# Kernel tuning notes

Hardware: AMD Instinct MI355X
Metric: run time of the kernel (lower is better)

Reference implementation:

```python
import jax, jax.numpy as jnp
import numpy as np

K = 5
TAU = 2.0
EPS = 1e-8
SLOPE = 0.2  # LeakyReLU negative slope
BASE = jnp.array([-2.0, -1.0, 0.0, 1.0, 2.0], dtype=jnp.float32)


def _leaky(x):
    return jnp.where(x >= 0, x, SLOPE * x)


def _bilinear1d(feat, x):
    """1D bilinear sample, equivalent to F.grid_sample on an [B,C,1,L] image
    with grid_y=0, padding_mode='border', align_corners=True.
    feat: [B,C,L], x: [B,M] normalized coords in [-1,1]. Returns [B,C,M]."""
    L = feat.shape[-1]
    ix = jnp.clip((x + 1.0) * 0.5 * (L - 1), 0.0, float(L - 1))  # border clamp
    x0 = jnp.floor(ix)
    w = (ix - x0)[:, None, :]  # [B,1,M]
    i0 = jnp.clip(x0.astype(jnp.int32), 0, L - 1)
    i1 = jnp.clip(i0 + 1, 0, L - 1)
    f0 = jnp.take_along_axis(feat, i0[:, None, :], axis=2)
    f1 = jnp.take_along_axis(feat, i1[:, None, :], axis=2)
    return f0 * (1.0 - w) + f1 * w


def setup_inputs() -> dict:
    key = jax.random.key(0)
    ks = jax.random.split(key, 10)
    B, C, Lin, N, H = 4, 256, 4096, 8192, 64
    out_dim = 1 + 1 + K + K  # 12
    feat_1d = jax.random.normal(ks[0], (B, C, Lin), dtype=jnp.float32)
    coords_1d = jax.random.uniform(ks[1], (B, N, 1), minval=-1.0, maxval=1.0, dtype=jnp.float32)
    cell_1d = jnp.full((B, N, 1), 2.0 / Lin, dtype=jnp.float32) * (1.0 + 0.1 * jax.random.uniform(ks[2], (B, N, 1)))
    in_dim = C + 2
    # NOTE: original zero-inits the last linear; we use small random weights to
    # exercise the full computation (non-degenerate offsets/gates).
    W1 = jax.random.normal(ks[3], (in_dim, H), dtype=jnp.float32) * (1.0 / np.sqrt(in_dim))
    b1 = jax.random.normal(ks[4], (H,), dtype=jnp.float32) * 0.01
    Wr = jax.random.normal(ks[5], (H, H), dtype=jnp.float32) * (1.0 / np.sqrt(H))
    br = jax.random.normal(ks[6], (H,), dtype=jnp.float32) * 0.01
    W3 = jax.random.normal(ks[7], (H, out_dim), dtype=jnp.float32) * 0.1
    b3 = jax.random.normal(ks[8], (out_dim,), dtype=jnp.float32) * 0.01
    return {"feat_1d": feat_1d, "coords_1d": coords_1d, "cell_1d": cell_1d,
            "W1": W1, "b1": b1, "Wr": Wr, "br": br, "W3": W3, "b3": b3}


def reference(feat_1d, coords_1d, cell_1d, W1, b1, Wr, br, W3, b3):
    B, C, Lin = feat_1d.shape
    N = coords_1d.shape[1]
    x = coords_1d[..., 0]  # [B,N]
    # anchor features at query coords
    f_anchor = _bilinear1d(feat_1d, x).transpose(0, 2, 1)  # [B,N,C]
    rin = jnp.concatenate([f_anchor, coords_1d, cell_1d], axis=-1)  # [B,N,C+2]
    # router MLP: Linear -> LeakyReLU -> ResidualBlock -> Linear
    h = _leaky(rin @ W1 + b1)
    h = _leaky(h + (h @ Wr + br))
    out = h @ W3 + b3  # [B,N,12]
    r_raw = out[..., 0:1]
    sigma_raw = out[..., 1:2]
    res_raw = out[..., 2:2 + K]
    gate_raw = out[..., 2 + K:2 + 2 * K]
    r = jnp.clip(jax.nn.softplus(r_raw) + 0.3, 0.3, 2.0)          # [B,N,1]
    sigma = jnp.clip(jax.nn.softplus(sigma_raw) + 0.5, 0.5, 3.0)  # [B,N,1]
    res = jnp.tanh(res_raw) * 0.5                                  # [B,N,K]
    off = r * BASE + res                                           # [B,N,K] pixel-unit offsets
    scale_x = 2.0 / max(Lin - 1, 1)
    deform_x = x[:, :, None] + off * scale_x                       # [B,N,K] normalized
    f = _bilinear1d(feat_1d, deform_x.reshape(B, N * K))           # [B,C,N*K]
    f = f.reshape(B, C, N, K).transpose(0, 2, 3, 1)                # [B,N,K,C]
    w_geo = jnp.exp(-0.5 * off ** 2 / ((sigma * TAU) ** 2 + EPS))  # [B,N,K]
    w = w_geo * jax.nn.sigmoid(gate_raw)
    w = w / (w.sum(axis=-1, keepdims=True) + EPS)
    out_feat = jnp.einsum('bnkc,bnk->bnc', f, w)                   # [B,N,C]
    return out_feat
```

## Files before the change

kernel.cpp:

```cpp
#include <hip/hip_runtime.h>
#include <math.h>

#define KK 5
#define C_DIM 256
#define LIN 4096
#define B_DIM 4
#define N_PTS 8192
#define PTS 32
#define NBUCK (B_DIM * LIN)
#define WROWS 32
#define SROWS 44
#define WPB (LIN / WROWS)

typedef short short8 __attribute__((ext_vector_type(8)));
typedef float f32x4  __attribute__((ext_vector_type(4)));

__device__ __forceinline__ float leaky(float v) { return v >= 0.0f ? v : 0.2f * v; }
__device__ __forceinline__ float softplus_f(float v) { return v > 20.0f ? v : log1pf(expf(v)); }
__device__ __forceinline__ float bflo(unsigned u) { return __uint_as_float(u << 16); }
__device__ __forceinline__ float bfhi(unsigned u) { return __uint_as_float(u & 0xFFFF0000u); }
__device__ __forceinline__ ushort f2bf(float f) {
    unsigned u = __float_as_uint(f);
    u += 0x7FFFu + ((u >> 16) & 1u);
    return (ushort)(u >> 16);
}
__device__ __forceinline__ float bf2f(ushort h) { return __uint_as_float((unsigned)h << 16); }
__device__ __forceinline__ int anchor_key(const float* coords, int pt) {
    float x = coords[pt];
    float ix = fminf(fmaxf((x + 1.0f) * 0.5f * (float)(LIN - 1), 0.0f), (float)(LIN - 1));
    return (pt >> 13) * LIN + (int)ix;
}

__global__ __launch_bounds__(256) void prep_weights(
    const float* __restrict__ W1, const float* __restrict__ Wr,
    ushort* __restrict__ W1t_hi, ushort* __restrict__ W1t_lo,
    ushort* __restrict__ Wrt_hi, ushort* __restrict__ Wrt_lo)
{
    int i = blockIdx.x * 256 + threadIdx.x;
    if (i < 64 * 264) {
        int j = i / 264, k = i % 264;
        float v = (k < 256) ? W1[(size_t)k * 64 + j] : 0.0f;
        ushort hi = f2bf(v);
        W1t_hi[i] = hi;
        W1t_lo[i] = f2bf(v - bf2f(hi));
    } else {
        int i2 = i - 64 * 264;
        if (i2 < 64 * 72) {
            int j = i2 / 72, k = i2 % 72;
            float v = (k < 64) ? Wr[(size_t)k * 64 + j] : 0.0f;
            ushort hi = f2bf(v);
            Wrt_hi[i2] = hi;
            Wrt_lo[i2] = f2bf(v - bf2f(hi));
        }
    }
}

__global__ __launch_bounds__(256) void sort_count(
    const float* __restrict__ coords, unsigned* __restrict__ hist)
{
    int pt = blockIdx.x * 256 + threadIdx.x;
    atomicAdd(&hist[anchor_key(coords, pt)], 1u);
}

__global__ __launch_bounds__(256) void sort_scan(
    const unsigned* __restrict__ hist, unsigned* __restrict__ offs,
    unsigned* __restrict__ pfx)
{
    __shared__ unsigned base[256];
    int t = threadIdx.x;
    unsigned s = 0;
    for (int i = 0; i < NBUCK / 256; i++) s += hist[t * (NBUCK / 256) + i];
    base[t] = s;
    __syncthreads();
    if (t == 0) {
        unsigned run = 0;
        for (int i = 0; i < 256; i++) { unsigned v = base[i]; base[i] = run; run += v; }
    }
    __syncthreads();
    unsigned run = base[t];
    for (int i = 0; i < NBUCK / 256; i++) {
        int idx = t * (NBUCK / 256) + i;
        offs[idx] = run;
        pfx[idx] = run;
        run += hist[idx];
    }
    if (t == 255) pfx[NBUCK] = run;
}

__global__ __launch_bounds__(256) void sort_scatter(
    const float* __restrict__ coords, unsigned* __restrict__ offs,
    int* __restrict__ perm)
{
    int pt = blockIdx.x * 256 + threadIdx.x;
    unsigned pos = atomicAdd(&offs[anchor_key(coords, pt)], 1u);
    perm[pos] = pt;
}

__global__ __launch_bounds__(256) void fused_kernel(
    const float* __restrict__ feat,
    const float* __restrict__ coords,
    const float* __restrict__ cell,
    const float* __restrict__ W1, const float* __restrict__ b1,
    const float* __restrict__ br,
    const float* __restrict__ W3, const float* __restrict__ b3,
    const ushort* __restrict__ W1t_hi, const ushort* __restrict__ W1t_lo,
    const ushort* __restrict__ Wrt_hi, const ushort* __restrict__ Wrt_lo,
    const int* __restrict__ perm, const unsigned* __restrict__ pfx,
    float* __restrict__ out)
{
    __shared__ ushort fs[SROWS][264];
    __shared__ ushort Ah[PTS][264], Al[PTS][264];
    __shared__ ushort H1h[PTS][72], H1l[PTS][72];
    __shared__ float  H2[PTS][68];
    __shared__ float  outs[PTS][12];
    __shared__ float  sxw[PTS][10];
    __shared__ float  xs[PTS], cls[PTS];
    __shared__ int    pts[PTS];

    const int t = threadIdx.x;
    const int b  = blockIdx.x / WPB;
    const int w0 = (blockIdx.x % WPB) * WROWS;
    const int rowLo = max(0, w0 - 5);
    const int rowHi = min(LIN, w0 + WROWS + 6);
    const int nrows = rowHi - rowLo;

    {
        const float* fsrc = feat + ((size_t)b * C_DIM + t) * LIN + rowLo;
        for (int l = 0; l < nrows; l++)
            fs[l][t] = f2bf(fsrc[l]);
    }

    const unsigned ptStart = pfx[b * LIN + w0];
    const unsigned ptEnd   = pfx[b * LIN + w0 + WROWS];

    const int wave = t >> 6, lane = t & 63;
    const int cr = lane & 15;
    const int kb = lane >> 4;
    const int jcol = wave * 16 + cr;
    const float wx  = W1[(size_t)256 * 64 + jcol];
    const float wc  = W1[(size_t)257 * 64 + jcol];
    const float bb1 = b1[jcol];
    const float brv = br[jcol];

    for (unsigned chunkBase = ptStart; chunkBase < ptEnd; chunkBase += PTS) {
        const int npts = (int)min((unsigned)PTS, ptEnd - chunkBase);
        __syncthreads();
        if (t < PTS) pts[t] = perm[chunkBase + min(t, npts - 1)];
        __syncthreads();

        {
            int p = t >> 3, l8 = t & 7;
            int pt = pts[p];
            float x = coords[pt];
            float ix = fminf(fmaxf((x + 1.0f) * 0.5f * (float)(LIN - 1), 0.0f), (float)(LIN - 1));
            float x0 = floorf(ix);
            int i0 = min((int)x0, LIN - 1);
            int i1 = min(i0 + 1, LIN - 1);
            float fr = ix - x0, om = 1.0f - fr;
            int r0 = i0 - rowLo, r1 = i1 - rowLo;
            if (l8 == 0) { xs[p] = x; cls[p] = cell[pt]; }
#pragma unroll
            for (int q = 0; q < 4; q++) {
                int c = l8 * 8 + q * 64;
                uint4 u0 = *(const uint4*)&fs[r0][c];
                uint4 u1 = *(const uint4*)&fs[r1][c];
                float v[8];
                v[0] = bflo(u0.x) * om + bflo(u1.x) * fr;
                v[1] = bfhi(u0.x) * om + bfhi(u1.x) * fr;
                v[2] = bflo(u0.y) * om + bflo(u1.y) * fr;
                v[3] = bfhi(u0.y) * om + bfhi(u1.y) * fr;
                v[4] = bflo(u0.z) * om + bflo(u1.z) * fr;
                v[5] = bfhi(u0.z) * om + bfhi(u1.z) * fr;
                v[6] = bflo(u0.w) * om + bflo(u1.w) * fr;
                v[7] = bfhi(u0.w) * om + bfhi(u1.w) * fr;
                ushort hv[8], lv[8];
#pragma unroll
                for (int e = 0; e < 8; e++) {
                    hv[e] = f2bf(v[e]);
                    lv[e] = f2bf(v[e] - bf2f(hv[e]));
                }
                *(uint4*)&Ah[p][c] = *(uint4*)hv;
                *(uint4*)&Al[p][c] = *(uint4*)lv;
            }
        }
        __syncthreads();

        f32x4 acc0 = {0.f, 0.f, 0.f, 0.f}, acc1 = acc0;
        {
            const ushort* B1h = W1t_hi + (size_t)jcol * 264;
            const ushort* B1l = W1t_lo + (size_t)jcol * 264;
#pragma unroll
            for (int k0 = 0; k0 < 256; k0 += 32) {
                int ko = k0 + kb * 8;
                short8 a0h = *(const short8*)&Ah[cr][ko];
                short8 a0l = *(const short8*)&Al[cr][ko];
                short8 a1h = *(const short8*)&Ah[16 + cr][ko];
                short8 a1l = *(const short8*)&Al[16 + cr][ko];
                short8 bh = *(const short8*)(B1h + ko);
                short8 bl = *(const short8*)(B1l + ko);
                acc0 = __builtin_amdgcn_mfma_f32_16x16x32_bf16(a0h, bh, acc0, 0, 0, 0);
                acc0 = __builtin_amdgcn_mfma_f32_16x16x32_bf16(a0h, bl, acc0, 0, 0, 0);
                acc0 = __builtin_amdgcn_mfma_f32_16x16x32_bf16(a0l, bh, acc0, 0, 0, 0);
                acc1 = __builtin_amdgcn_mfma_f32_16x16x32_bf16(a1h, bh, acc1, 0, 0, 0);
                acc1 = __builtin_amdgcn_mfma_f32_16x16x32_bf16(a1h, bl, acc1, 0, 0, 0);
                acc1 = __builtin_amdgcn_mfma_f32_16x16x32_bf16(a1l, bh, acc1, 0, 0, 0);
            }
        }
        float h1a[4], h1b[4];
#pragma unroll
        for (int r = 0; r < 4; r++) {
            int p0 = kb * 4 + r;
            float v0 = leaky(acc0[r] + xs[p0] * wx + cls[p0] * wc + bb1);
            h1a[r] = v0;
            ushort hi0 = f2bf(v0);
            H1h[p0][jcol] = hi0;
            H1l[p0][jcol] = f2bf(v0 - bf2f(hi0));
            int p1 = 16 + p0;
            float v1 = leaky(acc1[r] + xs[p1] * wx + cls[p1] * wc + bb1);
            h1b[r] = v1;
            ushort hi1 = f2bf(v1);
            H1h[p1][jcol] = hi1;
            H1l[p1][jcol] = f2bf(v1 - bf2f(hi1));
        }
        __syncthreads();

        {
            f32x4 r0 = {0.f, 0.f, 0.f, 0.f}, r1 = r0;
            const ushort* B2h = Wrt_hi + (size_t)jcol * 72;
            const ushort* B2l = Wrt_lo + (size_t)jcol * 72;
#pragma unroll
            for (int k0 = 0; k0 < 64; k0 += 32) {
                int ko = k0 + kb * 8;
                short8 a0h = *(const short8*)&H1h[cr][ko];
                short8 a0l = *(const short8*)&H1l[cr][ko];
                short8 a1h = *(const short8*)&H1h[16 + cr][ko];
                short8 a1l = *(const short8*)&H1l[16 + cr][ko];
                short8 bh = *(const short8*)(B2h + ko);
                short8 bl = *(const short8*)(B2l + ko);
                r0 = __builtin_amdgcn_mfma_f32_16x16x32_bf16(a0h, bh, r0, 0, 0, 0);
                r0 = __builtin_amdgcn_mfma_f32_16x16x32_bf16(a0h, bl, r0, 0, 0, 0);
                r0 = __builtin_amdgcn_mfma_f32_16x16x32_bf16(a0l, bh, r0, 0, 0, 0);
                r1 = __builtin_amdgcn_mfma_f32_16x16x32_bf16(a1h, bh, r1, 0, 0, 0);
                r1 = __builtin_amdgcn_mfma_f32_16x16x32_bf16(a1h, bl, r1, 0, 0, 0);
                r1 = __builtin_amdgcn_mfma_f32_16x16x32_bf16(a1l, bh, r1, 0, 0, 0);
            }
#pragma unroll
            for (int r = 0; r < 4; r++) {
                int p0 = kb * 4 + r;
                H2[p0][jcol]      = leaky(h1a[r] + r0[r] + brv);
                H2[16 + p0][jcol] = leaky(h1b[r] + r1[r] + brv);
            }
        }
        __syncthreads();

        {
            int p = t & 31;
            int o = t >> 5;
            for (int oo = o; oo < 12; oo += 8) {
                float acc = b3[oo];
#pragma unroll 4
                for (int l = 0; l < 64; l++)
                    acc = fmaf(H2[p][l], W3[(size_t)l * 12 + oo], acc);
                outs[p][oo] = acc;
            }
        }
        __syncthreads();

        if (t < PTS) {
            float x = xs[t];
            float r = softplus_f(outs[t][0]) + 0.3f;
            r = fminf(fmaxf(r, 0.3f), 2.0f);
            float sg = softplus_f(outs[t][1]) + 0.5f;
            sg = fminf(fmaxf(sg, 0.5f), 3.0f);
            float denom = (sg * 2.0f) * (sg * 2.0f) + 1e-8f;
            const float BASEv[KK] = {-2.0f, -1.0f, 0.0f, 1.0f, 2.0f};
            float wk[KK];
            float wsum = 0.0f;
#pragma unroll
            for (int k = 0; k < KK; k++) {
                float res = tanhf(outs[t][2 + k]) * 0.5f;
                float off = r * BASEv[k] + res;
                float dx = x + off * (2.0f / (float)(LIN - 1));
                float ix = (dx + 1.0f) * 0.5f * (float)(LIN - 1);
                ix = fminf(fmaxf(ix, 0.0f), (float)(LIN - 1));
                float gate = outs[t][2 + KK + k];
                float wgeo = expf(-0.5f * off * off / denom);
                float sig = 1.0f / (1.0f + expf(-gate));
                float w = wgeo * sig;
                sxw[t][k] = ix;
                wk[k] = w; wsum += w;
            }
            float inv = 1.0f / (wsum + 1e-8f);
#pragma unroll
            for (int k = 0; k < KK; k++) sxw[t][5 + k] = wk[k] * inv;
        }
        __syncthreads();

        {
            int worker = t >> 5, gl = t & 31;
            int c = gl * 8;
            for (int p = worker; p < npts; p += 8) {
                int pt = pts[p];
                float a0 = 0, a1 = 0, a2 = 0, a3 = 0, a4 = 0, a5 = 0, a6 = 0, a7 = 0;
#pragma unroll
                for (int k = 0; k < KK; k++) {
                    float ix = sxw[p][k];
                    float w  = sxw[p][5 + k];
                    float x0 = floorf(ix);
                    int i0 = (int)x0;
                    int i1 = min(i0 + 1, LIN - 1);
                    float fr = ix - x0;
                    uint4 u0 = *(const uint4*)&fs[i0 - rowLo][c];
                    uint4 u1 = *(const uint4*)&fs[i1 - rowLo][c];
                    float w0f = w * (1.0f - fr), w1f = w * fr;
                    a0 = fmaf(w0f, bflo(u0.x), fmaf(w1f, bflo(u1.x), a0));
                    a1 = fmaf(w0f, bfhi(u0.x), fmaf(w1f, bfhi(u1.x), a1));
                    a2 = fmaf(w0f, bflo(u0.y), fmaf(w1f, bflo(u1.y), a2));
                    a3 = fmaf(w0f, bfhi(u0.y), fmaf(w1f, bfhi(u1.y), a3));
                    a4 = fmaf(w0f, bflo(u0.z), fmaf(w1f, bflo(u1.z), a4));
                    a5 = fmaf(w0f, bfhi(u0.z), fmaf(w1f, bfhi(u1.z), a5));
                    a6 = fmaf(w0f, bflo(u0.w), fmaf(w1f, bflo(u1.w), a6));
                    a7 = fmaf(w0f, bfhi(u0.w), fmaf(w1f, bfhi(u1.w), a7));
                }
                float* op = out + (size_t)pt * C_DIM + c;
                *(float4*)op       = make_float4(a0, a1, a2, a3);
                *(float4*)(op + 4) = make_float4(a4, a5, a6, a7);
            }
        }
    }
}

extern "C" void kernel_launch(void* const* d_in, const int* in_sizes, int n_in,
                              void* d_out, int out_size, void* d_ws, size_t ws_size,
                              hipStream_t stream) {
    const float* feat   = (const float*)d_in[0];
    const float* coords = (const float*)d_in[1];
    const float* cell   = (const float*)d_in[2];
    const float* W1 = (const float*)d_in[3];
    const float* b1 = (const float*)d_in[4];
    const float* Wr = (const float*)d_in[5];
    const float* br = (const float*)d_in[6];
    const float* W3 = (const float*)d_in[7];
    const float* b3 = (const float*)d_in[8];
    float* out = (float*)d_out;

    char* ws = (char*)d_ws;
    ushort* W1t_hi = (ushort*)ws; ws += 64 * 264 * 2;
    ushort* W1t_lo = (ushort*)ws; ws += 64 * 264 * 2;
    ushort* Wrt_hi = (ushort*)ws; ws += 64 * 72 * 2;
    ushort* Wrt_lo = (ushort*)ws; ws += 64 * 72 * 2;
    ws = (char*)(((uintptr_t)ws + 255) & ~(uintptr_t)255);
    unsigned* hist = (unsigned*)ws; ws += NBUCK * 4;
    unsigned* offs = (unsigned*)ws; ws += NBUCK * 4;
    unsigned* pfx  = (unsigned*)ws; ws += (NBUCK + 1) * 4;
    ws = (char*)(((uintptr_t)ws + 255) & ~(uintptr_t)255);
    int* perm      = (int*)ws;      ws += (size_t)B_DIM * N_PTS * 4;

    int nPts = B_DIM * N_PTS;

    hipMemsetAsync(hist, 0, NBUCK * 4, stream);
    sort_count<<<nPts / 256, 256, 0, stream>>>(coords, hist);
    sort_scan<<<1, 256, 0, stream>>>(hist, offs, pfx);
    sort_scatter<<<nPts / 256, 256, 0, stream>>>(coords, offs, perm);

    prep_weights<<<(64 * 264 + 64 * 72 + 255) / 256, 256, 0, stream>>>(
        W1, Wr, W1t_hi, W1t_lo, Wrt_hi, Wrt_lo);

    fused_kernel<<<B_DIM * WPB, 256, 0, stream>>>(
        feat, coords, cell, W1, b1, br, W3, b3,
        W1t_hi, W1t_lo, Wrt_hi, Wrt_lo, perm, pfx, out);
}
```

Before: 148.4 us.

## Precompute first-layer GEMM on window rows and interpolate, coarsen sort buckets

Bilinear interpolation commutes with the first linear layer, so the first-layer MFMA GEMM now runs once per window on the stored feature rows. Each point then linearly interpolates the per-row results instead of running the 256-wide GEMM per point chunk. Windows shrink to 16 rows, which doubles the block count, and the sort now buckets by window with a merged scan+scatter kernel and fewer launches. LDS rows are padded and stored as hi/lo bf16 pairs. This adds a per-window GEMM whose cost is wasted on sparse windows, and the single-block scatter serialises 32K atomics.

After: 178.9 us. 20.6% more time.

```diff
diff --git a/kernel.cpp b/kernel.cpp
--- a/kernel.cpp
+++ b/kernel.cpp
@@ -7,36 +7,47 @@
 #define B_DIM 4
 #define N_PTS 8192
 #define PTS 32
-#define NBUCK (B_DIM * LIN)
-#define WROWS 32
-#define SROWS 44
+#define WROWS 16
 #define WPB (LIN / WROWS)
+#define NWIN (B_DIM * WPB)
+#define SROWS 28
+#define FS_STRIDE 268
+#define H1_STRIDE 76
+#define H2_STRIDE 67
+#define G_STRIDE 68
 
 typedef short short8 __attribute__((ext_vector_type(8)));
+typedef short short4v __attribute__((ext_vector_type(4)));
 typedef float f32x4  __attribute__((ext_vector_type(4)));
 
 __device__ __forceinline__ float leaky(float v) { return v >= 0.0f ? v : 0.2f * v; }
 __device__ __forceinline__ float softplus_f(float v) { return v > 20.0f ? v : log1pf(expf(v)); }
-__device__ __forceinline__ float bflo(unsigned u) { return __uint_as_float(u << 16); }
-__device__ __forceinline__ float bfhi(unsigned u) { return __uint_as_float(u & 0xFFFF0000u); }
 __device__ __forceinline__ ushort f2bf(float f) {
     unsigned u = __float_as_uint(f);
     u += 0x7FFFu + ((u >> 16) & 1u);
     return (ushort)(u >> 16);
 }
 __device__ __forceinline__ float bf2f(ushort h) { return __uint_as_float((unsigned)h << 16); }
-__device__ __forceinline__ int anchor_key(const float* coords, int pt) {
-    float x = coords[pt];
-    float ix = fminf(fmaxf((x + 1.0f) * 0.5f * (float)(LIN - 1), 0.0f), (float)(LIN - 1));
-    return (pt >> 13) * LIN + (int)ix;
-}
-
-__global__ __launch_bounds__(256) void prep_weights(
+
+__device__ __forceinline__ short8 lds_ld8(const ushort* p) {
+    union { short8 s8; short4v s4[2]; } u;
+    u.s4[0] = *(const short4v*)p;
+    u.s4[1] = *(const short4v*)(p + 4);
+    return u.s8;
+}
+
+__global__ __launch_bounds__(256) void prep_zero(
     const float* __restrict__ W1, const float* __restrict__ Wr,
     ushort* __restrict__ W1t_hi, ushort* __restrict__ W1t_lo,
-    ushort* __restrict__ Wrt_hi, ushort* __restrict__ Wrt_lo)
+    ushort* __restrict__ Wrt_hi, ushort* __restrict__ Wrt_lo,
+    unsigned* __restrict__ hist)
 {
-    int i = blockIdx.x * 256 + threadIdx.x;
+    int blk = blockIdx.x, t = threadIdx.x;
+    if (blk == 84) {
+        for (int i = t; i < NWIN; i += 256) hist[i] = 0u;
+        return;
+    }
+    int i = blk * 256 + t;
     if (i < 64 * 264) {
         int j = i / 264, k = i % 264;
         float v = (k < 256) ? W1[(size_t)k * 64 + j] : 0.0f;
@@ -58,209 +69,214 @@
 __global__ __launch_bounds__(256) void sort_count(
     const float* __restrict__ coords, unsigned* __restrict__ hist)
 {
-    int pt = blockIdx.x * 256 + threadIdx.x;
-    atomicAdd(&hist[anchor_key(coords, pt)], 1u);
-}
-
-__global__ __launch_bounds__(256) void sort_scan(
-    const unsigned* __restrict__ hist, unsigned* __restrict__ offs,
-    unsigned* __restrict__ pfx)
+    int gid = blockIdx.x * 256 + threadIdx.x;
+#pragma unroll
+    for (int i = 0; i < 4; i++) {
+        int pt = i * 8192 + gid;
+        float x = coords[pt];
+        float ix = fminf(fmaxf((x + 1.0f) * 0.5f * (float)(LIN - 1), 0.0f), (float)(LIN - 1));
+        int key = (pt >> 13) * WPB + ((int)ix >> 4);
+        atomicAdd(&hist[key], 1u);
+    }
+}
+
+__global__ __launch_bounds__(256) void scan_scatter(
+    const float* __restrict__ coords, const unsigned* __restrict__ hist,
+    unsigned* __restrict__ pfx, int* __restrict__ perm)
 {
-    __shared__ unsigned base[256];
+    __shared__ unsigned a[256];
+    __shared__ unsigned offs[NWIN];
     int t = threadIdx.x;
-    unsigned s = 0;
-    for (int i = 0; i < NBUCK / 256; i++) s += hist[t * (NBUCK / 256) + i];
-    base[t] = s;
+    unsigned h0 = hist[4 * t], h1 = hist[4 * t + 1];
+    unsigned h2 = hist[4 * t + 2], h3 = hist[4 * t + 3];
+    unsigned tsum = h0 + h1 + h2 + h3;
+    a[t] = tsum;
     __syncthreads();
-    if (t == 0) {
-        unsigned run = 0;
-        for (int i = 0; i < 256; i++) { unsigned v = base[i]; base[i] = run; run += v; }
-    }
+    for (int d = 1; d < 256; d <<= 1) {
+        unsigned v = (t >= d) ? a[t - d] : 0u;
+        __syncthreads();
+        a[t] += v;
+        __syncthreads();
+    }
+    unsigned ex = a[t] - tsum;
+    offs[4 * t]     = ex;
+    offs[4 * t + 1] = ex + h0;
+    offs[4 * t + 2] = ex + h0 + h1;
+    offs[4 * t + 3] = ex + h0 + h1 + h2;
+    pfx[4 * t]     = offs[4 * t];
+    pfx[4 * t + 1] = offs[4 * t + 1];
+    pfx[4 * t + 2] = offs[4 * t + 2];
+    pfx[4 * t + 3] = offs[4 * t + 3];
+    if (t == 255) pfx[NWIN] = a[255];
     __syncthreads();
-    unsigned run = base[t];
-    for (int i = 0; i < NBUCK / 256; i++) {
-        int idx = t * (NBUCK / 256) + i;
-        offs[idx] = run;
-        pfx[idx] = run;
-        run += hist[idx];
-    }
-    if (t == 255) pfx[NBUCK] = run;
-}
-
-__global__ __launch_bounds__(256) void sort_scatter(
-    const float* __restrict__ coords, unsigned* __restrict__ offs,
-    int* __restrict__ perm)
-{
-    int pt = blockIdx.x * 256 + threadIdx.x;
-    unsigned pos = atomicAdd(&offs[anchor_key(coords, pt)], 1u);
-    perm[pos] = pt;
-}
-
-__global__ __launch_bounds__(256) void fused_kernel(
-    const float* __restrict__ feat,
-    const float* __restrict__ coords,
+#pragma unroll 4
+    for (int i = 0; i < (B_DIM * N_PTS) / 256; i++) {
+        int pt = i * 256 + t;
+        float x = coords[pt];
+        float ix = fminf(fmaxf((x + 1.0f) * 0.5f * (float)(LIN - 1), 0.0f), (float)(LIN - 1));
+        int key = (pt >> 13) * WPB + ((int)ix >> 4);
+        unsigned pos = atomicAdd(&offs[key], 1u);
+        perm[pos] = pt;
+    }
+}
+
+__global__ __launch_bounds__(256, 3) void fused_kernel(
+    const float* __restrict__ feat, const float* __restrict__ coords,
     const float* __restrict__ cell,
     const float* __restrict__ W1, const float* __restrict__ b1,
-    const float* __restrict__ br,
-    const float* __restrict__ W3, const float* __restrict__ b3,
+    const float* __restrict__ br, const float* __restrict__ W3,
+    const float* __restrict__ b3,
     const ushort* __restrict__ W1t_hi, const ushort* __restrict__ W1t_lo,
     const ushort* __restrict__ Wrt_hi, const ushort* __restrict__ Wrt_lo,
     const int* __restrict__ perm, const unsigned* __restrict__ pfx,
     float* __restrict__ out)
 {
-    __shared__ ushort fs[SROWS][264];
-    __shared__ ushort Ah[PTS][264], Al[PTS][264];
-    __shared__ ushort H1h[PTS][72], H1l[PTS][72];
-    __shared__ float  H2[PTS][68];
+    __shared__ ushort fsh[SROWS * FS_STRIDE];
+    __shared__ __align__(16) char fslG_raw[SROWS * FS_STRIDE * 2];
+    ushort* fsl = (ushort*)fslG_raw;
+    float*  G   = (float*)fslG_raw;
+    __shared__ ushort H1h[PTS * H1_STRIDE], H1l[PTS * H1_STRIDE];
+    __shared__ float  H2[PTS * H2_STRIDE];
     __shared__ float  outs[PTS][12];
     __shared__ float  sxw[PTS][10];
-    __shared__ float  xs[PTS], cls[PTS];
-    __shared__ int    pts[PTS];
+    __shared__ float  xs[PTS], cls[PTS], frs[PTS];
+    __shared__ int    r0s[PTS], r1s[PTS], pts[PTS];
 
     const int t = threadIdx.x;
-    const int b  = blockIdx.x / WPB;
-    const int w0 = (blockIdx.x % WPB) * WROWS;
+    const int b   = blockIdx.x >> 8;
+    const int win = blockIdx.x & 255;
+    const int w0  = win * WROWS;
     const int rowLo = max(0, w0 - 5);
     const int rowHi = min(LIN, w0 + WROWS + 6);
     const int nrows = rowHi - rowLo;
 
     {
         const float* fsrc = feat + ((size_t)b * C_DIM + t) * LIN + rowLo;
-        for (int l = 0; l < nrows; l++)
-            fs[l][t] = f2bf(fsrc[l]);
-    }
-
-    const unsigned ptStart = pfx[b * LIN + w0];
-    const unsigned ptEnd   = pfx[b * LIN + w0 + WROWS];
-
-    const int wave = t >> 6, lane = t & 63;
-    const int cr = lane & 15;
-    const int kb = lane >> 4;
-    const int jcol = wave * 16 + cr;
-    const float wx  = W1[(size_t)256 * 64 + jcol];
-    const float wc  = W1[(size_t)257 * 64 + jcol];
-    const float bb1 = b1[jcol];
+#pragma unroll 4
+        for (int l = 0; l < nrows; l++) {
+            float v = fsrc[l];
+            ushort hi = f2bf(v);
+            fsh[l * FS_STRIDE + t] = hi;
+            fsl[l * FS_STRIDE + t] = f2bf(v - bf2f(hi));
+        }
+    }
+    __syncthreads();
+
+    const int lane = t & 63;
+    const int cr = lane & 15, kb = lane >> 4;
+    const int jcol = (t >> 6) * 16 + cr;
+
+    {
+        const int rA0 = min(cr, nrows - 1);
+        const int rA1 = min(16 + cr, nrows - 1);
+        const ushort* B1h = W1t_hi + (size_t)jcol * 264;
+        const ushort* B1l = W1t_lo + (size_t)jcol * 264;
+        f32x4 g0 = {0.f, 0.f, 0.f, 0.f}, g1 = g0;
+#pragma unroll
+        for (int k0 = 0; k0 < 256; k0 += 32) {
+            int ko = k0 + kb * 8;
+            short8 a0h = lds_ld8(fsh + rA0 * FS_STRIDE + ko);
+            short8 a0l = lds_ld8(fsl + rA0 * FS_STRIDE + ko);
+            short8 a1h = lds_ld8(fsh + rA1 * FS_STRIDE + ko);
+            short8 a1l = lds_ld8(fsl + rA1 * FS_STRIDE + ko);
+            short8 bh = *(const short8*)(B1h + ko);
+            short8 bl = *(const short8*)(B1l + ko);
+            g0 = __builtin_amdgcn_mfma_f32_16x16x32_bf16(a0h, bh, g0, 0, 0, 0);
+            g0 = __builtin_amdgcn_mfma_f32_16x16x32_bf16(a0h, bl, g0, 0, 0, 0);
+            g0 = __builtin_amdgcn_mfma_f32_16x16x32_bf16(a0l, bh, g0, 0, 0, 0);
+            g1 = __builtin_amdgcn_mfma_f32_16x16x32_bf16(a1h, bh, g1, 0, 0, 0);
+            g1 = __builtin_amdgcn_mfma_f32_16x16x32_bf16(a1h, bl, g1, 0, 0, 0);
+            g1 = __builtin_amdgcn_mfma_f32_16x16x32_bf16(a1l, bh, g1, 0, 0, 0);
+        }
+        __syncthreads();
+#pragma unroll
+        for (int r = 0; r < 4; r++) {
+            G[(kb * 4 + r) * G_STRIDE + jcol]        = g0[r];
+            G[(16 + kb * 4 + r) * G_STRIDE + jcol]   = g1[r];
+        }
+    }
+
+    const unsigned ptStart = pfx[b * WPB + win];
+    const unsigned ptEnd   = pfx[b * WPB + win + 1];
     const float brv = br[jcol];
 
-    for (unsigned chunkBase = ptStart; chunkBase < ptEnd; chunkBase += PTS) {
-        const int npts = (int)min((unsigned)PTS, ptEnd - chunkBase);
-        __syncthreads();
-        if (t < PTS) pts[t] = perm[chunkBase + min(t, npts - 1)];
-        __syncthreads();
-
-        {
-            int p = t >> 3, l8 = t & 7;
-            int pt = pts[p];
+    for (unsigned cb0 = ptStart; cb0 < ptEnd; cb0 += PTS) {
+        const int npts = (int)min((unsigned)PTS, ptEnd - cb0);
+        __syncthreads();
+        if (t < PTS) {
+            int pt = perm[cb0 + min(t, npts - 1)];
+            pts[t] = pt;
             float x = coords[pt];
             float ix = fminf(fmaxf((x + 1.0f) * 0.5f * (float)(LIN - 1), 0.0f), (float)(LIN - 1));
-            float x0 = floorf(ix);
-            int i0 = min((int)x0, LIN - 1);
+            float x0f = floorf(ix);
+            int i0 = min((int)x0f, LIN - 1);
             int i1 = min(i0 + 1, LIN - 1);
-            float fr = ix - x0, om = 1.0f - fr;
-            int r0 = i0 - rowLo, r1 = i1 - rowLo;
-            if (l8 == 0) { xs[p] = x; cls[p] = cell[pt]; }
-#pragma unroll
-            for (int q = 0; q < 4; q++) {
-                int c = l8 * 8 + q * 64;
-                uint4 u0 = *(const uint4*)&fs[r0][c];
-                uint4 u1 = *(const uint4*)&fs[r1][c];
-                float v[8];
-                v[0] = bflo(u0.x) * om + bflo(u1.x) * fr;
-                v[1] = bfhi(u0.x) * om + bfhi(u1.x) * fr;
-                v[2] = bflo(u0.y) * om + bflo(u1.y) * fr;
-                v[3] = bfhi(u0.y) * om + bfhi(u1.y) * fr;
-                v[4] = bflo(u0.z) * om + bflo(u1.z) * fr;
-                v[5] = bfhi(u0.z) * om + bfhi(u1.z) * fr;
-                v[6] = bflo(u0.w) * om + bflo(u1.w) * fr;
-                v[7] = bfhi(u0.w) * om + bfhi(u1.w) * fr;
-                ushort hv[8], lv[8];
-#pragma unroll
-                for (int e = 0; e < 8; e++) {
-                    hv[e] = f2bf(v[e]);
-                    lv[e] = f2bf(v[e] - bf2f(hv[e]));
-                }
-                *(uint4*)&Ah[p][c] = *(uint4*)hv;
-                *(uint4*)&Al[p][c] = *(uint4*)lv;
-            }
-        }
-        __syncthreads();
-
-        f32x4 acc0 = {0.f, 0.f, 0.f, 0.f}, acc1 = acc0;
+            r0s[t] = i0 - rowLo; r1s[t] = i1 - rowLo;
+            frs[t] = ix - x0f; xs[t] = x; cls[t] = cell[pt];
+        }
+        __syncthreads();
+
         {
-            const ushort* B1h = W1t_hi + (size_t)jcol * 264;
-            const ushort* B1l = W1t_lo + (size_t)jcol * 264;
-#pragma unroll
-            for (int k0 = 0; k0 < 256; k0 += 32) {
-                int ko = k0 + kb * 8;
-                short8 a0h = *(const short8*)&Ah[cr][ko];
-                short8 a0l = *(const short8*)&Al[cr][ko];
-                short8 a1h = *(const short8*)&Ah[16 + cr][ko];
-                short8 a1l = *(const short8*)&Al[16 + cr][ko];
-                short8 bh = *(const short8*)(B1h + ko);
-                short8 bl = *(const short8*)(B1l + ko);
-                acc0 = __builtin_amdgcn_mfma_f32_16x16x32_bf16(a0h, bh, acc0, 0, 0, 0);
-                acc0 = __builtin_amdgcn_mfma_f32_16x16x32_bf16(a0h, bl, acc0, 0, 0, 0);
-                acc0 = __builtin_amdgcn_mfma_f32_16x16x32_bf16(a0l, bh, acc0, 0, 0, 0);
-                acc1 = __builtin_amdgcn_mfma_f32_16x16x32_bf16(a1h, bh, acc1, 0, 0, 0);
-                acc1 = __builtin_amdgcn_mfma_f32_16x16x32_bf16(a1h, bl, acc1, 0, 0, 0);
-                acc1 = __builtin_amdgcn_mfma_f32_16x16x32_bf16(a1l, bh, acc1, 0, 0, 0);
-            }
-        }
-        float h1a[4], h1b[4];
-#pragma unroll
-        for (int r = 0; r < 4; r++) {
-            int p0 = kb * 4 + r;
-            float v0 = leaky(acc0[r] + xs[p0] * wx + cls[p0] * wc + bb1);
-            h1a[r] = v0;
-            ushort hi0 = f2bf(v0);
-            H1h[p0][jcol] = hi0;
-            H1l[p0][jcol] = f2bf(v0 - bf2f(hi0));
-            int p1 = 16 + p0;
-            float v1 = leaky(acc1[r] + xs[p1] * wx + cls[p1] * wc + bb1);
-            h1b[r] = v1;
-            ushort hi1 = f2bf(v1);
-            H1h[p1][jcol] = hi1;
-            H1l[p1][jcol] = f2bf(v1 - bf2f(hi1));
+            int p = t >> 3, j0 = (t & 7) * 8;
+            float fr = frs[p], om = 1.0f - fr;
+            float xv = xs[p], cv = cls[p];
+            const float* g0p = G + r0s[p] * G_STRIDE + j0;
+            const float* g1p = G + r1s[p] * G_STRIDE + j0;
+            const float* wxp = W1 + (size_t)256 * 64 + j0;
+            const float* wcp = W1 + (size_t)257 * 64 + j0;
+            const float* b1p = b1 + j0;
+            ushort* hh = H1h + p * H1_STRIDE + j0;
+            ushort* hl = H1l + p * H1_STRIDE + j0;
+#pragma unroll
+            for (int e = 0; e < 8; e++) {
+                float h = om * g0p[e] + fr * g1p[e] + xv * wxp[e] + cv * wcp[e] + b1p[e];
+                h = leaky(h);
+                ushort hi = f2bf(h);
+                hh[e] = hi;
+                hl[e] = f2bf(h - bf2f(hi));
+            }
         }
         __syncthreads();
 
         {
-            f32x4 r0 = {0.f, 0.f, 0.f, 0.f}, r1 = r0;
             const ushort* B2h = Wrt_hi + (size_t)jcol * 72;
             const ushort* B2l = Wrt_lo + (size_t)jcol * 72;
+            f32x4 r0a = {0.f, 0.f, 0.f, 0.f}, r1a = r0a;
 #pragma unroll
             for (int k0 = 0; k0 < 64; k0 += 32) {
                 int ko = k0 + kb * 8;
-                short8 a0h = *(const short8*)&H1h[cr][ko];
-                short8 a0l = *(const short8*)&H1l[cr][ko];
-                short8 a1h = *(const short8*)&H1h[16 + cr][ko];
-                short8 a1l = *(const short8*)&H1l[16 + cr][ko];
+                short8 a0h = lds_ld8(H1h + cr * H1_STRIDE + ko);
+                short8 a0l = lds_ld8(H1l + cr * H1_STRIDE + ko);
+                short8 a1h = lds_ld8(H1h + (16 + cr) * H1_STRIDE + ko);
+                short8 a1l = lds_ld8(H1l + (16 + cr) * H1_STRIDE + ko);
                 short8 bh = *(const short8*)(B2h + ko);
                 short8 bl = *(const short8*)(B2l + ko);
-                r0 = __builtin_amdgcn_mfma_f32_16x16x32_bf16(a0h, bh, r0, 0, 0, 0);
-                r0 = __builtin_amdgcn_mfma_f32_16x16x32_bf16(a0h, bl, r0, 0, 0, 0);
-                r0 = __builtin_amdgcn_mfma_f32_16x16x32_bf16(a0l, bh, r0, 0, 0, 0);
-                r1 = __builtin_amdgcn_mfma_f32_16x16x32_bf16(a1h, bh, r1, 0, 0, 0);
-                r1 = __builtin_amdgcn_mfma_f32_16x16x32_bf16(a1h, bl, r1, 0, 0, 0);
-                r1 = __builtin_amdgcn_mfma_f32_16x16x32_bf16(a1l, bh, r1, 0, 0, 0);
+                r0a = __builtin_amdgcn_mfma_f32_16x16x32_bf16(a0h, bh, r0a, 0, 0, 0);
+                r0a = __builtin_amdgcn_mfma_f32_16x16x32_bf16(a0h, bl, r0a, 0, 0, 0);
+                r0a = __builtin_amdgcn_mfma_f32_16x16x32_bf16(a0l, bh, r0a, 0, 0, 0);
+                r1a = __builtin_amdgcn_mfma_f32_16x16x32_bf16(a1h, bh, r1a, 0, 0, 0);
+                r1a = __builtin_amdgcn_mfma_f32_16x16x32_bf16(a1h, bl, r1a, 0, 0, 0);
+                r1a = __builtin_amdgcn_mfma_f32_16x16x32_bf16(a1l, bh, r1a, 0, 0, 0);
             }
 #pragma unroll
             for (int r = 0; r < 4; r++) {
                 int p0 = kb * 4 + r;
-                H2[p0][jcol]      = leaky(h1a[r] + r0[r] + brv);
-                H2[16 + p0][jcol] = leaky(h1b[r] + r1[r] + brv);
+                float h1v0 = bf2f(H1h[p0 * H1_STRIDE + jcol]) + bf2f(H1l[p0 * H1_STRIDE + jcol]);
+                H2[p0 * H2_STRIDE + jcol] = leaky(h1v0 + r0a[r] + brv);
+                int p1 = 16 + p0;
+                float h1v1 = bf2f(H1h[p1 * H1_STRIDE + jcol]) + bf2f(H1l[p1 * H1_STRIDE + jcol]);
+                H2[p1 * H2_STRIDE + jcol] = leaky(h1v1 + r1a[r] + brv);
             }
         }
         __syncthreads();
 
         {
-            int p = t & 31;
-            int o = t >> 5;
+            int p = t & 31, o = t >> 5;
             for (int oo = o; oo < 12; oo += 8) {
                 float acc = b3[oo];
-#pragma unroll 4
+#pragma unroll 8
                 for (int l = 0; l < 64; l++)
-                    acc = fmaf(H2[p][l], W3[(size_t)l * 12 + oo], acc);
+                    acc = fmaf(H2[p * H2_STRIDE + l], W3[(size_t)l * 12 + oo], acc);
                 outs[p][oo] = acc;
             }
         }
@@ -297,30 +313,33 @@
         __syncthreads();
 
         {
-            int worker = t >> 5, gl = t & 31;
+            int wg = t >> 5, gl = t & 31;
             int c = gl * 8;
-            for (int p = worker; p < npts; p += 8) {
+            for (int p = wg; p < npts; p += 8) {
                 int pt = pts[p];
                 float a0 = 0, a1 = 0, a2 = 0, a3 = 0, a4 = 0, a5 = 0, a6 = 0, a7 = 0;
 #pragma unroll
                 for (int k = 0; k < KK; k++) {
                     float ix = sxw[p][k];
                     float w  = sxw[p][5 + k];
-                    float x0 = floorf(ix);
-                    int i0 = (int)x0;
-                    int i1 = min(i0 + 1, LIN - 1);
-                    float fr = ix - x0;
-                    uint4 u0 = *(const uint4*)&fs[i0 - rowLo][c];
-                    uint4 u1 = *(const uint4*)&fs[i1 - rowLo][c];
+                    float x0f = floorf(ix);
+                    int i0 = (int)x0f;
+                    int rr0 = i0 - rowLo;
+                    int rr1 = min(i0 + 1, LIN - 1) - rowLo;
+                    float fr = ix - x0f;
+                    const ushort* q0 = fsh + rr0 * FS_STRIDE + c;
+                    const ushort* q1 = fsh + rr1 * FS_STRIDE + c;
+                    short4v u0a = *(const short4v*)q0, u0b = *(const short4v*)(q0 + 4);
+                    short4v u1a = *(const short4v*)q1, u1b = *(const short4v*)(q1 + 4);
                     float w0f = w * (1.0f - fr), w1f = w * fr;
-                    a0 = fmaf(w0f, bflo(u0.x), fmaf(w1f, bflo(u1.x), a0));
-                    a1 = fmaf(w0f, bfhi(u0.x), fmaf(w1f, bfhi(u1.x), a1));
-                    a2 = fmaf(w0f, bflo(u0.y), fmaf(w1f, bflo(u1.y), a2));
-                    a3 = fmaf(w0f, bfhi(u0.y), fmaf(w1f, bfhi(u1.y), a3));
-                    a4 = fmaf(w0f, bflo(u0.z), fmaf(w1f, bflo(u1.z), a4));
-                    a5 = fmaf(w0f, bfhi(u0.z), fmaf(w1f, bfhi(u1.z), a5));
-                    a6 = fmaf(w0f, bflo(u0.w), fmaf(w1f, bflo(u1.w), a6));
-                    a7 = fmaf(w0f, bfhi(u0.w), fmaf(w1f, bfhi(u1.w), a7));
+                    a0 = fmaf(w0f, bf2f((ushort)u0a[0]), fmaf(w1f, bf2f((ushort)u1a[0]), a0));
+                    a1 = fmaf(w0f, bf2f((ushort)u0a[1]), fmaf(w1f, bf2f((ushort)u1a[1]), a1));
+                    a2 = fmaf(w0f, bf2f((ushort)u0a[2]), fmaf(w1f, bf2f((ushort)u1a[2]), a2));
+                    a3 = fmaf(w0f, bf2f((ushort)u0a[3]), fmaf(w1f, bf2f((ushort)u1a[3]), a3));
+                    a4 = fmaf(w0f, bf2f((ushort)u0b[0]), fmaf(w1f, bf2f((ushort)u1b[0]), a4));
+                    a5 = fmaf(w0f, bf2f((ushort)u0b[1]), fmaf(w1f, bf2f((ushort)u1b[1]), a5));
+                    a6 = fmaf(w0f, bf2f((ushort)u0b[2]), fmaf(w1f, bf2f((ushort)u1b[2]), a6));
+                    a7 = fmaf(w0f, bf2f((ushort)u0b[3]), fmaf(w1f, bf2f((ushort)u1b[3]), a7));
                 }
                 float* op = out + (size_t)pt * C_DIM + c;
                 *(float4*)op       = make_float4(a0, a1, a2, a3);
@@ -350,23 +369,15 @@
     ushort* Wrt_hi = (ushort*)ws; ws += 64 * 72 * 2;
     ushort* Wrt_lo = (ushort*)ws; ws += 64 * 72 * 2;
     ws = (char*)(((uintptr_t)ws + 255) & ~(uintptr_t)255);
-    unsigned* hist = (unsigned*)ws; ws += NBUCK * 4;
-    unsigned* offs = (unsigned*)ws; ws += NBUCK * 4;
-    unsigned* pfx  = (unsigned*)ws; ws += (NBUCK + 1) * 4;
+    unsigned* hist = (unsigned*)ws; ws += NWIN * 4;
+    unsigned* pfx  = (unsigned*)ws; ws += (NWIN + 1) * 4;
     ws = (char*)(((uintptr_t)ws + 255) & ~(uintptr_t)255);
     int* perm      = (int*)ws;      ws += (size_t)B_DIM * N_PTS * 4;
 
-    int nPts = B_DIM * N_PTS;
-
-    hipMemsetAsync(hist, 0, NBUCK * 4, stream);
-    sort_count<<<nPts / 256, 256, 0, stream>>>(coords, hist);
-    sort_scan<<<1, 256, 0, stream>>>(hist, offs, pfx);
-    sort_scatter<<<nPts / 256, 256, 0, stream>>>(coords, offs, perm);
-
-    prep_weights<<<(64 * 264 + 64 * 72 + 255) / 256, 256, 0, stream>>>(
-        W1, Wr, W1t_hi, W1t_lo, Wrt_hi, Wrt_lo);
-
-    fused_kernel<<<B_DIM * WPB, 256, 0, stream>>>(
+    prep_zero<<<85, 256, 0, stream>>>(W1, Wr, W1t_hi, W1t_lo, Wrt_hi, Wrt_lo, hist);
+    sort_count<<<32, 256, 0, stream>>>(coords, hist);
+    scan_scatter<<<1, 256, 0, stream>>>(coords, hist, pfx, perm);
+    fused_kernel<<<NWIN, 256, 0, stream>>>(
         feat, coords, cell, W1, b1, br, W3, b3,
         W1t_hi, W1t_lo, Wrt_hi, Wrt_lo, perm, pfx, out);
 }
```
